# Optimization experiments

Measured on AMD Instinct MI355X. Metric: run time of the kernel, lower is better.

Reference implementation:

```python
import jax, jax.numpy as jnp
import numpy as np

N_NODES = 100_000
N_EDGES = 1_600_000
N_GRAPHS = 512
D_IN = 128
D_H = 64
D_OUT = 32
N_CONV = 4  # n_layers - 1
BN_EPS = 1e-5


def setup_inputs() -> dict:
    key = jax.random.key(0)
    ks = jax.random.split(key, 10)
    h = jax.random.normal(ks[0], (N_NODES, D_IN), dtype=jnp.float32)
    src = jax.random.randint(ks[1], (N_EDGES,), 0, N_NODES, dtype=jnp.int32)
    dst = jax.random.randint(ks[2], (N_EDGES,), 0, N_NODES, dtype=jnp.int32)
    graph_ids = jnp.sort(jax.random.randint(ks[3], (N_NODES,), 0, N_GRAPHS, dtype=jnp.int32))
    s = 0.05
    fc1_w0 = jax.random.normal(ks[4], (D_IN, D_H), dtype=jnp.float32) * s
    fc1_w = jax.random.normal(ks[5], (N_CONV - 1, D_H, D_H), dtype=jnp.float32) * s
    fc2_w = jax.random.normal(ks[6], (N_CONV, D_H, D_H), dtype=jnp.float32) * s
    bn1_g = jnp.ones((N_CONV, D_H), dtype=jnp.float32)
    bn1_b = jnp.zeros((N_CONV, D_H), dtype=jnp.float32)
    bn2_g = jnp.ones((N_CONV, D_H), dtype=jnp.float32)
    bn2_b = jnp.zeros((N_CONV, D_H), dtype=jnp.float32)
    pred_w = jax.random.normal(ks[7], (N_CONV, D_H, D_OUT), dtype=jnp.float32) * s
    pred_b = jnp.zeros((N_CONV, D_OUT), dtype=jnp.float32)
    return {"h": h, "src": src, "dst": dst, "graph_ids": graph_ids,
            "fc1_w0": fc1_w0, "fc1_w": fc1_w, "fc2_w": fc2_w,
            "bn1_g": bn1_g, "bn1_b": bn1_b, "bn2_g": bn2_g, "bn2_b": bn2_b,
            "pred_w": pred_w, "pred_b": pred_b}


def _batch_norm(x, g, b):
    # PyTorch training-mode BN: batch mean, biased variance
    m = jnp.mean(x, axis=0)
    v = jnp.var(x, axis=0)
    return (x - m) * jax.lax.rsqrt(v + BN_EPS) * g + b


def reference(h, src, dst, graph_ids, fc1_w0, fc1_w, fc2_w,
              bn1_g, bn1_b, bn2_g, bn2_b, pred_w, pred_b):
    # GIN: h' = MLP((1+eps)*h + sum_{j in N(i)} h_j), eps=0 (learn_eps=False)
    score = jnp.zeros((N_GRAPHS, D_OUT), dtype=h.dtype)
    for l in range(N_CONV):
        agg = h + jax.ops.segment_sum(h[src], dst, num_segments=N_NODES)
        w1 = fc1_w0 if l == 0 else fc1_w[l - 1]
        # _MLP: fc2(relu(BN(fc1(x))))
        h = jax.nn.relu(_batch_norm(agg @ w1, bn1_g[l], bn1_b[l])) @ fc2_w[l]
        # outer BN + relu
        h = jax.nn.relu(_batch_norm(h, bn2_g[l], bn2_b[l]))
        # SumPooling per graph; readout skips layer-0 input rep, dropout is eval-mode identity
        pooled = jax.ops.segment_sum(h, graph_ids, num_segments=N_GRAPHS)
        score = score + pooled @ pred_w[l] + pred_b[l]
    return score
```

## Files before the change

### kernel.cpp

```cpp
#include <hip/hip_runtime.h>

#define N_NODES 100000
#define N_EDGES 1600000
#define N_GRAPHS 512
#define D_IN 128
#define D_H 64
#define D_OUT 32
#define N_CONV 4
#define BN_EPS 1e-5f
#define NSLOT 32

#define NB 512
#define NPB 196
#define NBUSED 511
#define CHUNK 8192
#define MAXE 4096

typedef unsigned short ushort_t;
typedef unsigned int uint_t;
typedef __attribute__((ext_vector_type(8))) short bf16x8;
typedef __attribute__((ext_vector_type(4))) float f32x4;
union U4B8 { uint4 u; bf16x8 v; };

__device__ inline float b2f(ushort_t u) {
    union { uint_t i; float f; } c; c.i = ((uint_t)u) << 16; return c.f;
}
__device__ inline ushort_t f2b(float f) {
    union { uint_t i; float f; } c; c.f = f;
    uint_t r = (c.i + 0x7fffu + ((c.i >> 16) & 1u)) >> 16;
    return (ushort_t)r;
}
__device__ inline float blo(uint_t v) { return b2f((ushort_t)(v & 0xffffu)); }
__device__ inline float bhi(uint_t v) { return b2f((ushort_t)(v >> 16)); }

__global__ __launch_bounds__(256) void zero_kernel(int* __restrict__ p, int nwords) {
    int i = blockIdx.x * 256 + threadIdx.x;
    if (i < nwords) p[i] = 0;
}

__global__ __launch_bounds__(256) void bucket_count(const int* __restrict__ dst,
                                                    int* __restrict__ bucketCnt) {
    __shared__ int l[NB];
    int t = threadIdx.x;
    for (int i = t; i < NB; i += 256) l[i] = 0;
    __syncthreads();
    long base = (long)blockIdx.x * 4096;
    for (int i = t; i < 4096; i += 256) {
        long e = base + i;
        if (e < N_EDGES) atomicAdd(&l[(unsigned)dst[e] / NPB], 1);
    }
    __syncthreads();
    for (int i = t; i < NB; i += 256) if (l[i]) atomicAdd(&bucketCnt[i], l[i]);
}

__global__ __launch_bounds__(512) void bucket_scan(const int* __restrict__ bucketCnt,
                                                   int* __restrict__ bucketOffs,
                                                   int* __restrict__ bucketCur) {
    __shared__ int s[512];
    int t = threadIdx.x;
    int v = bucketCnt[t];
    s[t] = v;
    __syncthreads();
    for (int off = 1; off < 512; off <<= 1) {
        int u = (t >= off) ? s[t - off] : 0;
        __syncthreads();
        s[t] += u;
        __syncthreads();
    }
    int excl = s[t] - v;
    bucketOffs[t] = excl;
    bucketCur[t] = excl;
    if (t == 511) bucketOffs[512] = s[511];
}

__global__ __launch_bounds__(256) void binned_scatter(const int* __restrict__ src,
                                                      const int* __restrict__ dst,
                                                      int* __restrict__ bucketCur,
                                                      uint2* __restrict__ pairs) {
    __shared__ uint2 sorted[CHUNK];
    __shared__ int lcnt[NB], loffs[NB], lcur[NB], gbase[NB];
    __shared__ int ps[256];
    int t = threadIdx.x;
    long e0 = (long)blockIdx.x * CHUNK;
    int nvalid = (int)min((long)CHUNK, (long)N_EDGES - e0);
    for (int i = t; i < NB; i += 256) lcnt[i] = 0;
    __syncthreads();
    for (int i = t; i < nvalid; i += 256)
        atomicAdd(&lcnt[(unsigned)dst[e0 + i] / NPB], 1);
    __syncthreads();
    int a0 = lcnt[2 * t], a1 = lcnt[2 * t + 1];
    ps[t] = a0 + a1;
    __syncthreads();
    for (int off = 1; off < 256; off <<= 1) {
        int u = (t >= off) ? ps[t - off] : 0;
        __syncthreads();
        ps[t] += u;
        __syncthreads();
    }
    int ex = ps[t] - (a0 + a1);
    loffs[2 * t] = ex; loffs[2 * t + 1] = ex + a0;
    lcur[2 * t] = ex;  lcur[2 * t + 1] = ex + a0;
    __syncthreads();
    for (int i = t; i < NB; i += 256) {
        int c = lcnt[i];
        gbase[i] = c ? atomicAdd(&bucketCur[i], c) : 0;
    }
    for (int i = t; i < nvalid; i += 256) {
        int d = dst[e0 + i];
        int b = (unsigned)d / NPB;
        int pos = atomicAdd(&lcur[b], 1);
        sorted[pos] = make_uint2((unsigned)src[e0 + i], (unsigned)d);
    }
    __syncthreads();
    for (int i = t; i < nvalid; i += 256) {
        uint2 pr = sorted[i];
        int b = pr.y / NPB;
        long gpos = (long)gbase[b] + (i - loffs[b]);
        pairs[gpos] = pr;
    }
}

__global__ __launch_bounds__(256) void csr_finalize(const uint2* __restrict__ pairs,
                                                    const int* __restrict__ bucketOffs,
                                                    int* __restrict__ offs,
                                                    int* __restrict__ csr) {
    __shared__ uint2 lp[MAXE];
    __shared__ int lsrc[MAXE];
    __shared__ int lcnt[NPB], lofs[NPB + 1], lcur[NPB];
    __shared__ int ls[256];
    int b = blockIdx.x, t = threadIdx.x;
    int e0 = bucketOffs[b], e1 = bucketOffs[b + 1];
    int ne = e1 - e0;
    int n0 = b * NPB;
    int nn = min(NPB, N_NODES - n0);
    for (int i = t; i < ne; i += 256) lp[i] = pairs[e0 + i];
    for (int i = t; i < nn; i += 256) lcnt[i] = 0;
    __syncthreads();
    for (int i = t; i < ne; i += 256) atomicAdd(&lcnt[lp[i].y - n0], 1);
    __syncthreads();
    int v = (t < nn) ? lcnt[t] : 0;
    ls[t] = v;
    __syncthreads();
    for (int off = 1; off < 256; off <<= 1) {
        int u = (t >= off) ? ls[t - off] : 0;
        __syncthreads();
        ls[t] += u;
        __syncthreads();
    }
    if (t < nn) { lofs[t] = ls[t] - v; lcur[t] = ls[t] - v; offs[n0 + t] = e0 + ls[t] - v; }
    if (t == 0 && b == NBUSED - 1) offs[N_NODES] = e1;
    __syncthreads();
    for (int i = t; i < ne; i += 256) {
        int pos = atomicAdd(&lcur[lp[i].y - n0], 1);
        lsrc[pos] = (int)lp[i].x;
    }
    __syncthreads();
    for (int i = t; i < ne; i += 256) csr[e0 + i] = lsrc[i];
}

#define SLABS 4
#define GEMM_BLOCKS 391
__global__ __launch_bounds__(256) void gemm0(const float* __restrict__ in,
                                             const float* __restrict__ w,
                                             ushort_t* __restrict__ y16) {
    __shared__ uint4 Bl[4][4][64];
    int t = threadIdx.x;
    for (int idx = t; idx < 4 * 4 * 64; idx += 256) {
        int l = idx & 63, nt = (idx >> 6) & 3, kk = idx >> 8;
        int k0 = kk * 32 + ((l >> 4) << 3), c = nt * 16 + (l & 15);
        uint4 o;
        o.x = (uint_t)f2b(w[(k0 + 0) * 64 + c]) | ((uint_t)f2b(w[(k0 + 1) * 64 + c]) << 16);
        o.y = (uint_t)f2b(w[(k0 + 2) * 64 + c]) | ((uint_t)f2b(w[(k0 + 3) * 64 + c]) << 16);
        o.z = (uint_t)f2b(w[(k0 + 4) * 64 + c]) | ((uint_t)f2b(w[(k0 + 5) * 64 + c]) << 16);
        o.w = (uint_t)f2b(w[(k0 + 6) * 64 + c]) | ((uint_t)f2b(w[(k0 + 7) * 64 + c]) << 16);
        Bl[kk][nt][l] = o;
    }
    __syncthreads();
    int wv = t >> 6, lane = t & 63, lq = lane >> 4, lr = lane & 15;
    bf16x8 B[4][4];
#pragma unroll
    for (int kk = 0; kk < 4; kk++)
#pragma unroll
        for (int nt = 0; nt < 4; nt++) { U4B8 cv; cv.u = Bl[kk][nt][lane]; B[kk][nt] = cv.v; }
    for (int s = 0; s < SLABS; s++) {
        long rb = ((long)blockIdx.x * SLABS + s) * 64 + wv * 16;
        long n = rb + lr;
        const float* rp = in + (n < N_NODES ? n : 0) * 128;
        f32x4 zero = {0.f, 0.f, 0.f, 0.f};
        f32x4 acc[4] = {zero, zero, zero, zero};
#pragma unroll
        for (int kk = 0; kk < 4; kk++) {
            float4 u = *(const float4*)(rp + kk * 32 + lq * 8);
            float4 v = *(const float4*)(rp + kk * 32 + lq * 8 + 4);
            bf16x8 a;
            a[0] = (short)f2b(u.x); a[1] = (short)f2b(u.y);
            a[2] = (short)f2b(u.z); a[3] = (short)f2b(u.w);
            a[4] = (short)f2b(v.x); a[5] = (short)f2b(v.y);
            a[6] = (short)f2b(v.z); a[7] = (short)f2b(v.w);
#pragma unroll
            for (int nt = 0; nt < 4; nt++)
                acc[nt] = __builtin_amdgcn_mfma_f32_16x16x32_bf16(a, B[kk][nt], acc[nt], 0, 0, 0);
        }
#pragma unroll
        for (int nt = 0; nt < 4; nt++)
#pragma unroll
            for (int j = 0; j < 4; j++) {
                long rr = rb + lq * 4 + j;
                if (rr < N_NODES) y16[rr * 64 + nt * 16 + lr] = f2b(acc[nt][j]);
            }
    }
}

template <bool OSTAT>
__global__ __launch_bounds__(256) void gemm_bn(const uint4* __restrict__ in,
                                               const float* __restrict__ w,
                                               const float* __restrict__ bnip,
                                               const float* __restrict__ gi,
                                               const float* __restrict__ bi,
                                               ushort_t* __restrict__ outY,
                                               float* __restrict__ ostat) {
    __shared__ uint4 Bl[2][4][64];
    __shared__ float sc[64], sh[64];
    __shared__ float red1[4][64], red2[4][64];
    int t = threadIdx.x;
    if (t < 64) {
        float S = 0.f, S2 = 0.f;
        for (int s = 0; s < NSLOT; s++) { S += bnip[s * 128 + t]; S2 += bnip[s * 128 + 64 + t]; }
        float mean = S * (1.f / N_NODES);
        float var = S2 * (1.f / N_NODES) - mean * mean;
        float r = rsqrtf(var + BN_EPS);
        float scv = gi[t] * r;
        sc[t] = scv; sh[t] = bi[t] - mean * scv;
    }
    for (int idx = t; idx < 2 * 4 * 64; idx += 256) {
        int l = idx & 63, nt = (idx >> 6) & 3, kk = idx >> 8;
        int k0 = kk * 32 + ((l >> 4) << 3), c = nt * 16 + (l & 15);
        uint4 o;
        o.x = (uint_t)f2b(w[(k0 + 0) * 64 + c]) | ((uint_t)f2b(w[(k0 + 1) * 64 + c]) << 16);
        o.y = (uint_t)f2b(w[(k0 + 2) * 64 + c]) | ((uint_t)f2b(w[(k0 + 3) * 64 + c]) << 16);
        o.z = (uint_t)f2b(w[(k0 + 4) * 64 + c]) | ((uint_t)f2b(w[(k0 + 5) * 64 + c]) << 16);
        o.w = (uint_t)f2b(w[(k0 + 6) * 64 + c]) | ((uint_t)f2b(w[(k0 + 7) * 64 + c]) << 16);
        Bl[kk][nt][l] = o;
    }
    __syncthreads();
    int wv = t >> 6, lane = t & 63, lq = lane >> 4, lr = lane & 15;
    bf16x8 B[2][4];
#pragma unroll
    for (int kk = 0; kk < 2; kk++)
#pragma unroll
        for (int nt = 0; nt < 4; nt++) { U4B8 cv; cv.u = Bl[kk][nt][lane]; B[kk][nt] = cv.v; }
    float s1[4] = {0.f, 0.f, 0.f, 0.f}, s2[4] = {0.f, 0.f, 0.f, 0.f};
    for (int s = 0; s < SLABS; s++) {
        long rb = ((long)blockIdx.x * SLABS + s) * 64 + wv * 16;
        long n = rb + lr;
        bool ok = n < N_NODES;
        const uint4* rp = in + (ok ? n : 0) * 8;
        f32x4 zero = {0.f, 0.f, 0.f, 0.f};
        f32x4 acc[4] = {zero, zero, zero, zero};
#pragma unroll
        for (int kk = 0; kk < 2; kk++) {
            bf16x8 a;
            if (ok) {
                uint4 v = rp[kk * 4 + lq];
                int k0 = kk * 32 + lq * 8;
                float x0 = fmaxf(blo(v.x) * sc[k0 + 0] + sh[k0 + 0], 0.f);
                float x1 = fmaxf(bhi(v.x) * sc[k0 + 1] + sh[k0 + 1], 0.f);
                float x2 = fmaxf(blo(v.y) * sc[k0 + 2] + sh[k0 + 2], 0.f);
                float x3 = fmaxf(bhi(v.y) * sc[k0 + 3] + sh[k0 + 3], 0.f);
                float x4 = fmaxf(blo(v.z) * sc[k0 + 4] + sh[k0 + 4], 0.f);
                float x5 = fmaxf(bhi(v.z) * sc[k0 + 5] + sh[k0 + 5], 0.f);
                float x6 = fmaxf(blo(v.w) * sc[k0 + 6] + sh[k0 + 6], 0.f);
                float x7 = fmaxf(bhi(v.w) * sc[k0 + 7] + sh[k0 + 7], 0.f);
                a[0] = (short)f2b(x0); a[1] = (short)f2b(x1);
                a[2] = (short)f2b(x2); a[3] = (short)f2b(x3);
                a[4] = (short)f2b(x4); a[5] = (short)f2b(x5);
                a[6] = (short)f2b(x6); a[7] = (short)f2b(x7);
            } else {
#pragma unroll
                for (int j = 0; j < 8; j++) a[j] = 0;
            }
#pragma unroll
            for (int nt = 0; nt < 4; nt++)
                acc[nt] = __builtin_amdgcn_mfma_f32_16x16x32_bf16(a, B[kk][nt], acc[nt], 0, 0, 0);
        }
#pragma unroll
        for (int nt = 0; nt < 4; nt++)
#pragma unroll
            for (int j = 0; j < 4; j++) {
                long rr = rb + lq * 4 + j;
                float val = acc[nt][j];
                if (rr < N_NODES) outY[rr * 64 + nt * 16 + lr] = f2b(val);
                if (OSTAT) { s1[nt] += val; s2[nt] += val * val; }
            }
    }
    if (OSTAT) {
#pragma unroll
        for (int nt = 0; nt < 4; nt++) {
            s1[nt] += __shfl_xor(s1[nt], 16); s1[nt] += __shfl_xor(s1[nt], 32);
            s2[nt] += __shfl_xor(s2[nt], 16); s2[nt] += __shfl_xor(s2[nt], 32);
        }
        if (lq == 0) {
#pragma unroll
            for (int nt = 0; nt < 4; nt++) {
                red1[wv][nt * 16 + lr] = s1[nt];
                red2[wv][nt * 16 + lr] = s2[nt];
            }
        }
        __syncthreads();
        if (t < 64) {
            float S = red1[0][t] + red1[1][t] + red1[2][t] + red1[3][t];
            float S2 = red2[0][t] + red2[1][t] + red2[2][t] + red2[3][t];
            int slot = blockIdx.x & (NSLOT - 1);
            atomicAdd(&ostat[slot * 128 + t], S);
            atomicAdd(&ostat[slot * 128 + 64 + t], S2);
        }
    }
}

__global__ __launch_bounds__(256) void aggregate(const uint_t* __restrict__ y32,
                                                 const int* __restrict__ offs,
                                                 const int* __restrict__ csr,
                                                 uint_t* __restrict__ aggOut,
                                                 float* __restrict__ bn1p) {
    int t = threadIdx.x;
    int wv = t >> 6, lane = t & 63;
    int g = lane >> 3, l = lane & 7;
    __shared__ float l1[4][64], l2[4][64];
    float st1[8], st2[8];
#pragma unroll
    for (int m = 0; m < 8; m++) { st1[m] = 0.f; st2[m] = 0.f; }
    int nb_base = blockIdx.x * 32 + wv * 8;
    for (int j = 0; j < 8; j++) {
        int n = nb_base + j;
        if (n >= N_NODES) break;
        int p0 = offs[n], p1 = offs[n + 1];
        int cnt = 1 + (p1 - p0);
        int rounds = (cnt + 7) >> 3;
        float accA[4] = {0.f, 0.f, 0.f, 0.f}, accB[4] = {0.f, 0.f, 0.f, 0.f};
        int e = g;
        int idx = (e == 0) ? n : ((e < cnt) ? csr[p0 + e - 1] : -1);
        for (int r = 0; r < rounds; r++) {
            int ne = e + 8;
            int nidx = (r + 1 < rounds && ne < cnt) ? csr[p0 + ne - 1] : -1;
            if (idx >= 0) {
                uint4 v = *(const uint4*)(y32 + (long)idx * 32 + 4 * l);
                accA[0] += __uint_as_float(v.x << 16);
                accB[0] += __uint_as_float(v.x & 0xffff0000u);
                accA[1] += __uint_as_float(v.y << 16);
                accB[1] += __uint_as_float(v.y & 0xffff0000u);
                accA[2] += __uint_as_float(v.z << 16);
                accB[2] += __uint_as_float(v.z & 0xffff0000u);
                accA[3] += __uint_as_float(v.w << 16);
                accB[3] += __uint_as_float(v.w & 0xffff0000u);
            }
            e = ne; idx = nidx;
        }
#pragma unroll
        for (int m = 0; m < 4; m++) {
            accA[m] += __shfl_xor(accA[m], 8);
            accB[m] += __shfl_xor(accB[m], 8);
            accA[m] += __shfl_xor(accA[m], 16);
            accB[m] += __shfl_xor(accB[m], 16);
            accA[m] += __shfl_xor(accA[m], 32);
            accB[m] += __shfl_xor(accB[m], 32);
        }
        if (g == 0) {
            uint4 o;
            o.x = (uint_t)f2b(accA[0]) | ((uint_t)f2b(accB[0]) << 16);
            o.y = (uint_t)f2b(accA[1]) | ((uint_t)f2b(accB[1]) << 16);
            o.z = (uint_t)f2b(accA[2]) | ((uint_t)f2b(accB[2]) << 16);
            o.w = (uint_t)f2b(accA[3]) | ((uint_t)f2b(accB[3]) << 16);
            *(uint4*)&aggOut[(long)n * 32 + 4 * l] = o;
            st1[0] += accA[0]; st2[0] += accA[0] * accA[0];
            st1[1] += accB[0]; st2[1] += accB[0] * accB[0];
            st1[2] += accA[1]; st2[2] += accA[1] * accA[1];
            st1[3] += accB[1]; st2[3] += accB[1] * accB[1];
            st1[4] += accA[2]; st2[4] += accA[2] * accA[2];
            st1[5] += accB[2]; st2[5] += accB[2] * accB[2];
            st1[6] += accA[3]; st2[6] += accA[3] * accA[3];
            st1[7] += accB[3]; st2[7] += accB[3] * accB[3];
        }
    }
    if (g == 0) {
#pragma unroll
        for (int m = 0; m < 8; m++) { l1[wv][8 * l + m] = st1[m]; l2[wv][8 * l + m] = st2[m]; }
    }
    __syncthreads();
    if (t < 64) {
        float S = l1[0][t] + l1[1][t] + l1[2][t] + l1[3][t];
        float S2 = l2[0][t] + l2[1][t] + l2[2][t] + l2[3][t];
        int slot = blockIdx.x & (NSLOT - 1);
        atomicAdd(&bn1p[slot * 128 + t], S);
        atomicAdd(&bn1p[slot * 128 + 64 + t], S2);
    }
}

__global__ __launch_bounds__(256) void bn_pool(const uint_t* __restrict__ h2,
                                               const float* __restrict__ bn2p,
                                               const float* __restrict__ g2,
                                               const float* __restrict__ b2,
                                               const int* __restrict__ gid,
                                               float* __restrict__ pooled) {
    __shared__ float sc[64], sh[64];
    int t = threadIdx.x;
    if (t < 64) {
        float S = 0.f, S2 = 0.f;
        for (int s = 0; s < NSLOT; s++) { S += bn2p[s * 128 + t]; S2 += bn2p[s * 128 + 64 + t]; }
        float mean = S * (1.f / N_NODES);
        float var = S2 * (1.f / N_NODES) - mean * mean;
        float r = rsqrtf(var + BN_EPS);
        float scv = g2[t] * r;
        sc[t] = scv; sh[t] = b2[t] - mean * scv;
    }
    __syncthreads();
    int c = t & 31, rs = t >> 5;
    float sA = sc[2 * c], hA = sh[2 * c], sB = sc[2 * c + 1], hB = sh[2 * c + 1];
    long base = (long)blockIdx.x * 256;
    float pa = 0.f, pb2 = 0.f; int gc = -1;
    for (int i = 0; i < 32; i++) {
        long n = base + rs + 8 * i;
        if (n >= N_NODES) break;
        int g = gid[n];
        uint_t v = h2[n * 32 + c];
        float x0 = fmaxf(blo(v) * sA + hA, 0.f);
        float x1 = fmaxf(bhi(v) * sB + hB, 0.f);
        if (g != gc) {
            if (gc >= 0) {
                atomicAdd(&pooled[(long)gc * 64 + 2 * c], pa);
                atomicAdd(&pooled[(long)gc * 64 + 2 * c + 1], pb2);
            }
            gc = g; pa = 0.f; pb2 = 0.f;
        }
        pa += x0; pb2 += x1;
    }
    if (gc >= 0) {
        atomicAdd(&pooled[(long)gc * 64 + 2 * c], pa);
        atomicAdd(&pooled[(long)gc * 64 + 2 * c + 1], pb2);
    }
}

__global__ __launch_bounds__(256) void score_kernel(const float* __restrict__ pooled,
                                                    const float* __restrict__ pw,
                                                    const float* __restrict__ pb,
                                                    float* __restrict__ out) {
    int idx = blockIdx.x * 256 + threadIdx.x;
    int g = idx >> 5, o = idx & 31;
    float acc = 0.f;
    for (int l = 0; l < N_CONV; l++) {
        acc += pb[l * 32 + o];
        const float* pr = pooled + (long)l * N_GRAPHS * 64 + (long)g * 64;
        const float* wr = pw + l * 64 * 32;
        for (int k = 0; k < 64; k++) acc += pr[k] * wr[k * 32 + o];
    }
    out[idx] = acc;
}

extern "C" void kernel_launch(void* const* d_in, const int* in_sizes, int n_in,
                              void* d_out, int out_size, void* d_ws, size_t ws_size,
                              hipStream_t stream) {
    const float* h     = (const float*)d_in[0];
    const int*   src   = (const int*)d_in[1];
    const int*   dst   = (const int*)d_in[2];
    const int*   gid   = (const int*)d_in[3];
    const float* fc1w0 = (const float*)d_in[4];
    const float* fc1w  = (const float*)d_in[5];
    const float* fc2w  = (const float*)d_in[6];
    const float* bn1g  = (const float*)d_in[7];
    const float* bn1b  = (const float*)d_in[8];
    const float* bn2g  = (const float*)d_in[9];
    const float* bn2b  = (const float*)d_in[10];
    const float* pw    = (const float*)d_in[11];
    const float* pb    = (const float*)d_in[12];
    float* out = (float*)d_out;

    char* ws = (char*)d_ws;
    uint_t*   AGG16   = (uint_t*)  (ws);
    uint2*    pairs   = (uint2*)   (ws);
    ushort_t* X16     = (ushort_t*)(ws + 25600000);
    ushort_t* Y16     = (ushort_t*)(ws + 38400000);
    float*    bnst    = (float*)   (ws + 51200000);
    float*    pooled  = (float*)   (ws + 51331072);
    int*   bucketCnt  = (int*)     (ws + 51855360);
    int*   bucketOffs = (int*)     (ws + 51857408);
    int*   bucketCur  = (int*)     (ws + 51859460);
    int*   offs       = (int*)     (ws + 51861508);
    int*   csr        = (int*)     (ws + 52261512);

    const int zwords = (51857408 - 51200000) / 4;
    zero_kernel<<<(zwords + 255) / 256, 256, 0, stream>>>((int*)bnst, zwords);

    bucket_count<<<(N_EDGES + 4095) / 4096, 256, 0, stream>>>(dst, bucketCnt);
    bucket_scan<<<1, 512, 0, stream>>>(bucketCnt, bucketOffs, bucketCur);
    binned_scatter<<<(N_EDGES + CHUNK - 1) / CHUNK, 256, 0, stream>>>(src, dst, bucketCur, pairs);
    csr_finalize<<<NBUSED, 256, 0, stream>>>(pairs, bucketOffs, offs, csr);

    for (int l = 0; l < N_CONV; l++) {
        float* bn1p = bnst + (long)l * 8192;
        float* bn2p = bn1p + 4096;
        float* pl = pooled + (long)l * N_GRAPHS * 64;
        if (l == 0) {
            gemm0<<<GEMM_BLOCKS, 256, 0, stream>>>(h, fc1w0, Y16);
        } else {
            float* bn2p_prev = bnst + (long)(l - 1) * 8192 + 4096;
            gemm_bn<false><<<GEMM_BLOCKS, 256, 0, stream>>>((const uint4*)X16,
                fc1w + (long)(l - 1) * 4096, bn2p_prev,
                bn2g + (l - 1) * 64, bn2b + (l - 1) * 64, Y16, (float*)nullptr);
        }
        aggregate<<<3125, 256, 0, stream>>>((const uint_t*)Y16, offs, csr, AGG16, bn1p);
        gemm_bn<true><<<GEMM_BLOCKS, 256, 0, stream>>>((const uint4*)AGG16,
            fc2w + (long)l * 4096, bn1p, bn1g + l * 64, bn1b + l * 64, X16, bn2p);
        bn_pool<<<391, 256, 0, stream>>>((const uint_t*)X16, bn2p, bn2g + l * 64,
                                         bn2b + l * 64, gid, pl);
    }
    score_kernel<<<64, 256, 0, stream>>>(pooled, pw, pb, out);
}
```

Baseline: 410.8 us.

## Fuse pooling into next-layer GEMM, pack CSR pairs, prefetch aggregate gathers

For layers 0-2 the per-graph sum pooling moves into the next layer's gemm_bn prologue. That kernel already computes the BN+ReLU activations, so it adds them into an LDS pool buffer and flushes with global atomics, which removes three bn_pool launches and their reread of X16. The CSR build packs each (src, local dst) pair into one 32-bit word, halving pairs traffic and LDS use. The aggregate kernel becomes grid-stride over 2048 blocks and software-prefetches the next neighbour row. The per-element LDS atomics in the GEMM prologue add contention, and the pooled sums accumulate in a different order than before.

```diff
diff --git a/kernel.cpp b/kernel.cpp
--- a/kernel.cpp
+++ b/kernel.cpp
@@ -15,6 +15,8 @@
 #define NBUSED 511
 #define CHUNK 8192
 #define MAXE 4096
+#define AGG_BLOCKS 2048
+#define AGG_CHUNKS 3125
 
 typedef unsigned short ushort_t;
 typedef unsigned int uint_t;
@@ -76,8 +78,9 @@
 __global__ __launch_bounds__(256) void binned_scatter(const int* __restrict__ src,
                                                       const int* __restrict__ dst,
                                                       int* __restrict__ bucketCur,
-                                                      uint2* __restrict__ pairs) {
-    __shared__ uint2 sorted[CHUNK];
+                                                      uint_t* __restrict__ pairs) {
+    __shared__ uint_t sortedp[CHUNK];
+    __shared__ ushort_t sbkt[CHUNK];
     __shared__ int lcnt[NB], loffs[NB], lcur[NB], gbase[NB];
     __shared__ int ps[256];
     int t = threadIdx.x;
@@ -109,24 +112,24 @@
         int d = dst[e0 + i];
         int b = (unsigned)d / NPB;
         int pos = atomicAdd(&lcur[b], 1);
-        sorted[pos] = make_uint2((unsigned)src[e0 + i], (unsigned)d);
+        sortedp[pos] = ((uint_t)src[e0 + i] << 9) | (uint_t)(d - b * NPB);
+        sbkt[pos] = (ushort_t)b;
     }
     __syncthreads();
     for (int i = t; i < nvalid; i += 256) {
-        uint2 pr = sorted[i];
-        int b = pr.y / NPB;
+        int b = sbkt[i];
         long gpos = (long)gbase[b] + (i - loffs[b]);
-        pairs[gpos] = pr;
-    }
-}
-
-__global__ __launch_bounds__(256) void csr_finalize(const uint2* __restrict__ pairs,
+        pairs[gpos] = sortedp[i];
+    }
+}
+
+__global__ __launch_bounds__(256) void csr_finalize(const uint_t* __restrict__ pairs,
                                                     const int* __restrict__ bucketOffs,
                                                     int* __restrict__ offs,
                                                     int* __restrict__ csr) {
-    __shared__ uint2 lp[MAXE];
+    __shared__ uint_t lp[MAXE];
     __shared__ int lsrc[MAXE];
-    __shared__ int lcnt[NPB], lofs[NPB + 1], lcur[NPB];
+    __shared__ int lcnt[NPB], lcur[NPB];
     __shared__ int ls[256];
     int b = blockIdx.x, t = threadIdx.x;
     int e0 = bucketOffs[b], e1 = bucketOffs[b + 1];
@@ -136,7 +139,7 @@
     for (int i = t; i < ne; i += 256) lp[i] = pairs[e0 + i];
     for (int i = t; i < nn; i += 256) lcnt[i] = 0;
     __syncthreads();
-    for (int i = t; i < ne; i += 256) atomicAdd(&lcnt[lp[i].y - n0], 1);
+    for (int i = t; i < ne; i += 256) atomicAdd(&lcnt[lp[i] & 511u], 1);
     __syncthreads();
     int v = (t < nn) ? lcnt[t] : 0;
     ls[t] = v;
@@ -147,12 +150,13 @@
         ls[t] += u;
         __syncthreads();
     }
-    if (t < nn) { lofs[t] = ls[t] - v; lcur[t] = ls[t] - v; offs[n0 + t] = e0 + ls[t] - v; }
+    if (t < nn) { lcur[t] = ls[t] - v; offs[n0 + t] = e0 + ls[t] - v; }
     if (t == 0 && b == NBUSED - 1) offs[N_NODES] = e1;
     __syncthreads();
     for (int i = t; i < ne; i += 256) {
-        int pos = atomicAdd(&lcur[lp[i].y - n0], 1);
-        lsrc[pos] = (int)lp[i].x;
+        uint_t p = lp[i];
+        int pos = atomicAdd(&lcur[p & 511u], 1);
+        lsrc[pos] = (int)(p >> 9);
     }
     __syncthreads();
     for (int i = t; i < ne; i += 256) csr[e0 + i] = lsrc[i];
@@ -211,17 +215,20 @@
     }
 }
 
-template <bool OSTAT>
+template <bool OSTAT, bool POOL>
 __global__ __launch_bounds__(256) void gemm_bn(const uint4* __restrict__ in,
                                                const float* __restrict__ w,
                                                const float* __restrict__ bnip,
                                                const float* __restrict__ gi,
                                                const float* __restrict__ bi,
                                                ushort_t* __restrict__ outY,
-                                               float* __restrict__ ostat) {
+                                               float* __restrict__ ostat,
+                                               const int* __restrict__ gid,
+                                               float* __restrict__ pooledPrev) {
     __shared__ uint4 Bl[2][4][64];
     __shared__ float sc[64], sh[64];
     __shared__ float red1[4][64], red2[4][64];
+    __shared__ float lds_pool[8][64];
     int t = threadIdx.x;
     if (t < 64) {
         float S = 0.f, S2 = 0.f;
@@ -231,6 +238,9 @@
         float r = rsqrtf(var + BN_EPS);
         float scv = gi[t] * r;
         sc[t] = scv; sh[t] = bi[t] - mean * scv;
+    }
+    if (POOL) {
+        for (int i = t; i < 8 * 64; i += 256) lds_pool[i >> 6][i & 63] = 0.f;
     }
     for (int idx = t; idx < 2 * 4 * 64; idx += 256) {
         int l = idx & 63, nt = (idx >> 6) & 3, kk = idx >> 8;
@@ -244,6 +254,7 @@
     }
     __syncthreads();
     int wv = t >> 6, lane = t & 63, lq = lane >> 4, lr = lane & 15;
+    int g_base = POOL ? gid[blockIdx.x * 256] : 0;
     bf16x8 B[2][4];
 #pragma unroll
     for (int kk = 0; kk < 2; kk++)
@@ -255,6 +266,8 @@
         long n = rb + lr;
         bool ok = n < N_NODES;
         const uint4* rp = in + (ok ? n : 0) * 8;
+        int gl = 0;
+        if (POOL && ok) gl = gid[n] - g_base;
         f32x4 zero = {0.f, 0.f, 0.f, 0.f};
         f32x4 acc[4] = {zero, zero, zero, zero};
 #pragma unroll
@@ -271,6 +284,28 @@
                 float x5 = fmaxf(bhi(v.z) * sc[k0 + 5] + sh[k0 + 5], 0.f);
                 float x6 = fmaxf(blo(v.w) * sc[k0 + 6] + sh[k0 + 6], 0.f);
                 float x7 = fmaxf(bhi(v.w) * sc[k0 + 7] + sh[k0 + 7], 0.f);
+                if (POOL) {
+                    if (gl < 8) {
+                        atomicAdd(&lds_pool[gl][k0 + 0], x0);
+                        atomicAdd(&lds_pool[gl][k0 + 1], x1);
+                        atomicAdd(&lds_pool[gl][k0 + 2], x2);
+                        atomicAdd(&lds_pool[gl][k0 + 3], x3);
+                        atomicAdd(&lds_pool[gl][k0 + 4], x4);
+                        atomicAdd(&lds_pool[gl][k0 + 5], x5);
+                        atomicAdd(&lds_pool[gl][k0 + 6], x6);
+                        atomicAdd(&lds_pool[gl][k0 + 7], x7);
+                    } else {
+                        long pb = (long)(g_base + gl) * 64 + k0;
+                        atomicAdd(&pooledPrev[pb + 0], x0);
+                        atomicAdd(&pooledPrev[pb + 1], x1);
+                        atomicAdd(&pooledPrev[pb + 2], x2);
+                        atomicAdd(&pooledPrev[pb + 3], x3);
+                        atomicAdd(&pooledPrev[pb + 4], x4);
+                        atomicAdd(&pooledPrev[pb + 5], x5);
+                        atomicAdd(&pooledPrev[pb + 6], x6);
+                        atomicAdd(&pooledPrev[pb + 7], x7);
+                    }
+                }
                 a[0] = (short)f2b(x0); a[1] = (short)f2b(x1);
                 a[2] = (short)f2b(x2); a[3] = (short)f2b(x3);
                 a[4] = (short)f2b(x4); a[5] = (short)f2b(x5);
@@ -315,6 +350,17 @@
             atomicAdd(&ostat[slot * 128 + 64 + t], S2);
         }
     }
+    if (POOL) {
+        __syncthreads();
+        for (int i = t; i < 8 * 64; i += 256) {
+            float v = lds_pool[i >> 6][i & 63];
+            if (v != 0.f) {
+                int gg = g_base + (i >> 6);
+                if (gg < N_GRAPHS)
+                    atomicAdd(&pooledPrev[(long)gg * 64 + (i & 63)], v);
+            }
+        }
+    }
 }
 
 __global__ __launch_bounds__(256) void aggregate(const uint_t* __restrict__ y32,
@@ -329,56 +375,60 @@
     float st1[8], st2[8];
 #pragma unroll
     for (int m = 0; m < 8; m++) { st1[m] = 0.f; st2[m] = 0.f; }
-    int nb_base = blockIdx.x * 32 + wv * 8;
-    for (int j = 0; j < 8; j++) {
-        int n = nb_base + j;
-        if (n >= N_NODES) break;
-        int p0 = offs[n], p1 = offs[n + 1];
-        int cnt = 1 + (p1 - p0);
-        int rounds = (cnt + 7) >> 3;
-        float accA[4] = {0.f, 0.f, 0.f, 0.f}, accB[4] = {0.f, 0.f, 0.f, 0.f};
-        int e = g;
-        int idx = (e == 0) ? n : ((e < cnt) ? csr[p0 + e - 1] : -1);
-        for (int r = 0; r < rounds; r++) {
-            int ne = e + 8;
-            int nidx = (r + 1 < rounds && ne < cnt) ? csr[p0 + ne - 1] : -1;
-            if (idx >= 0) {
-                uint4 v = *(const uint4*)(y32 + (long)idx * 32 + 4 * l);
-                accA[0] += __uint_as_float(v.x << 16);
-                accB[0] += __uint_as_float(v.x & 0xffff0000u);
-                accA[1] += __uint_as_float(v.y << 16);
-                accB[1] += __uint_as_float(v.y & 0xffff0000u);
-                accA[2] += __uint_as_float(v.z << 16);
-                accB[2] += __uint_as_float(v.z & 0xffff0000u);
-                accA[3] += __uint_as_float(v.w << 16);
-                accB[3] += __uint_as_float(v.w & 0xffff0000u);
-            }
-            e = ne; idx = nidx;
-        }
-#pragma unroll
-        for (int m = 0; m < 4; m++) {
-            accA[m] += __shfl_xor(accA[m], 8);
-            accB[m] += __shfl_xor(accB[m], 8);
-            accA[m] += __shfl_xor(accA[m], 16);
-            accB[m] += __shfl_xor(accB[m], 16);
-            accA[m] += __shfl_xor(accA[m], 32);
-            accB[m] += __shfl_xor(accB[m], 32);
-        }
-        if (g == 0) {
-            uint4 o;
-            o.x = (uint_t)f2b(accA[0]) | ((uint_t)f2b(accB[0]) << 16);
-            o.y = (uint_t)f2b(accA[1]) | ((uint_t)f2b(accB[1]) << 16);
-            o.z = (uint_t)f2b(accA[2]) | ((uint_t)f2b(accB[2]) << 16);
-            o.w = (uint_t)f2b(accA[3]) | ((uint_t)f2b(accB[3]) << 16);
-            *(uint4*)&aggOut[(long)n * 32 + 4 * l] = o;
-            st1[0] += accA[0]; st2[0] += accA[0] * accA[0];
-            st1[1] += accB[0]; st2[1] += accB[0] * accB[0];
-            st1[2] += accA[1]; st2[2] += accA[1] * accA[1];
-            st1[3] += accB[1]; st2[3] += accB[1] * accB[1];
-            st1[4] += accA[2]; st2[4] += accA[2] * accA[2];
-            st1[5] += accB[2]; st2[5] += accB[2] * accB[2];
-            st1[6] += accA[3]; st2[6] += accA[3] * accA[3];
-            st1[7] += accB[3]; st2[7] += accB[3] * accB[3];
+    for (int chunk = blockIdx.x; chunk < AGG_CHUNKS; chunk += AGG_BLOCKS) {
+        int nb_base = chunk * 32 + wv * 8;
+        for (int j = 0; j < 8; j++) {
+            int n = nb_base + j;
+            int p0 = offs[n], p1 = offs[n + 1];
+            int cnt = 1 + (p1 - p0);
+            int rounds = (cnt + 7) >> 3;
+            float accA[4] = {0.f, 0.f, 0.f, 0.f}, accB[4] = {0.f, 0.f, 0.f, 0.f};
+            int e = g;
+            int idx = (g == 0) ? n : ((g < cnt) ? csr[p0 + g - 1] : -1);
+            uint4 v;
+            if (idx >= 0) v = *(const uint4*)(y32 + (long)idx * 32 + 4 * l);
+            for (int r = 0; r < rounds; r++) {
+                int ne = e + 8;
+                int nidx = (ne < cnt) ? csr[p0 + ne - 1] : -1;
+                uint4 vn;
+                if (nidx >= 0) vn = *(const uint4*)(y32 + (long)nidx * 32 + 4 * l);
+                if (idx >= 0) {
+                    accA[0] += __uint_as_float(v.x << 16);
+                    accB[0] += __uint_as_float(v.x & 0xffff0000u);
+                    accA[1] += __uint_as_float(v.y << 16);
+                    accB[1] += __uint_as_float(v.y & 0xffff0000u);
+                    accA[2] += __uint_as_float(v.z << 16);
+                    accB[2] += __uint_as_float(v.z & 0xffff0000u);
+                    accA[3] += __uint_as_float(v.w << 16);
+                    accB[3] += __uint_as_float(v.w & 0xffff0000u);
+                }
+                e = ne; idx = nidx; v = vn;
+            }
+#pragma unroll
+            for (int m = 0; m < 4; m++) {
+                accA[m] += __shfl_xor(accA[m], 8);
+                accB[m] += __shfl_xor(accB[m], 8);
+                accA[m] += __shfl_xor(accA[m], 16);
+                accB[m] += __shfl_xor(accB[m], 16);
+                accA[m] += __shfl_xor(accA[m], 32);
+                accB[m] += __shfl_xor(accB[m], 32);
+            }
+            if (g == 0) {
+                uint4 o;
+                o.x = (uint_t)f2b(accA[0]) | ((uint_t)f2b(accB[0]) << 16);
+                o.y = (uint_t)f2b(accA[1]) | ((uint_t)f2b(accB[1]) << 16);
+                o.z = (uint_t)f2b(accA[2]) | ((uint_t)f2b(accB[2]) << 16);
+                o.w = (uint_t)f2b(accA[3]) | ((uint_t)f2b(accB[3]) << 16);
+                *(uint4*)&aggOut[(long)n * 32 + 4 * l] = o;
+                st1[0] += accA[0]; st2[0] += accA[0] * accA[0];
+                st1[1] += accB[0]; st2[1] += accB[0] * accB[0];
+                st1[2] += accA[1]; st2[2] += accA[1] * accA[1];
+                st1[3] += accB[1]; st2[3] += accB[1] * accB[1];
+                st1[4] += accA[2]; st2[4] += accA[2] * accA[2];
+                st1[5] += accB[2]; st2[5] += accB[2] * accB[2];
+                st1[6] += accA[3]; st2[6] += accA[3] * accA[3];
+                st1[7] += accB[3]; st2[7] += accB[3] * accB[3];
+            }
         }
     }
     if (g == 0) {
@@ -475,7 +525,7 @@
 
     char* ws = (char*)d_ws;
     uint_t*   AGG16   = (uint_t*)  (ws);
-    uint2*    pairs   = (uint2*)   (ws);
+    uint_t*   pairs   = (uint_t*)  (ws);
     ushort_t* X16     = (ushort_t*)(ws + 25600000);
     ushort_t* Y16     = (ushort_t*)(ws + 38400000);
     float*    bnst    = (float*)   (ws + 51200000);
@@ -497,20 +547,23 @@
     for (int l = 0; l < N_CONV; l++) {
         float* bn1p = bnst + (long)l * 8192;
         float* bn2p = bn1p + 4096;
-        float* pl = pooled + (long)l * N_GRAPHS * 64;
         if (l == 0) {
             gemm0<<<GEMM_BLOCKS, 256, 0, stream>>>(h, fc1w0, Y16);
         } else {
             float* bn2p_prev = bnst + (long)(l - 1) * 8192 + 4096;
-            gemm_bn<false><<<GEMM_BLOCKS, 256, 0, stream>>>((const uint4*)X16,
+            float* pl_prev = pooled + (long)(l - 1) * N_GRAPHS * 64;
+            gemm_bn<false, true><<<GEMM_BLOCKS, 256, 0, stream>>>((const uint4*)X16,
                 fc1w + (long)(l - 1) * 4096, bn2p_prev,
-                bn2g + (l - 1) * 64, bn2b + (l - 1) * 64, Y16, (float*)nullptr);
-        }
-        aggregate<<<3125, 256, 0, stream>>>((const uint_t*)Y16, offs, csr, AGG16, bn1p);
-        gemm_bn<true><<<GEMM_BLOCKS, 256, 0, stream>>>((const uint4*)AGG16,
-            fc2w + (long)l * 4096, bn1p, bn1g + l * 64, bn1b + l * 64, X16, bn2p);
-        bn_pool<<<391, 256, 0, stream>>>((const uint_t*)X16, bn2p, bn2g + l * 64,
-                                         bn2b + l * 64, gid, pl);
-    }
+                bn2g + (l - 1) * 64, bn2b + (l - 1) * 64, Y16,
+                (float*)nullptr, gid, pl_prev);
+        }
+        aggregate<<<AGG_BLOCKS, 256, 0, stream>>>((const uint_t*)Y16, offs, csr, AGG16, bn1p);
+        gemm_bn<true, false><<<GEMM_BLOCKS, 256, 0, stream>>>((const uint4*)AGG16,
+            fc2w + (long)l * 4096, bn1p, bn1g + l * 64, bn1b + l * 64, X16, bn2p,
+            (const int*)nullptr, (float*)nullptr);
+    }
+    bn_pool<<<391, 256, 0, stream>>>((const uint_t*)X16,
+        bnst + 3 * 8192 + 4096, bn2g + 3 * 64, bn2b + 3 * 64, gid,
+        pooled + 3L * N_GRAPHS * 64);
     score_kernel<<<64, 256, 0, stream>>>(pooled, pw, pb, out);
 }
```

Result: slower. 509.2 us (+24.0%).
